# Kernel tuning notes

Measured on AMD Instinct MI355X. Metric: run time of the kernel, lower is better.

The kernel has to match this reference:

```python
import jax, jax.numpy as jnp
import numpy as np
import math

NUM_CLASSES = 722
BLUR_RANGE = 3
# gaussian_val(dist, sigma=1) = exp(-2**dist / (2 * 2**1)) = exp(-2**dist / 4)
DECAYS = [math.exp(-(2.0 ** d) / 4.0) for d in range(BLUR_RANGE + 1)]


def setup_inputs() -> dict:
    key = jax.random.key(0)
    k1, k2 = jax.random.split(key)
    pred = jax.random.normal(k1, (32, 2048, NUM_CLASSES), dtype=jnp.float32)
    target = jax.random.randint(k2, (32, 2048), 0, NUM_CLASSES, dtype=jnp.int32)
    return {"pred": pred, "target": target}


def _smoothed_label(target):
    # target: (b, t) int -> (b, t, C) float32 gaussian-blurred one-hot.
    b, t = target.shape
    bi = jnp.arange(b)[:, None]   # (b, 1)
    ti = jnp.arange(t)[None, :]   # (1, t)
    one_hot = jnp.zeros((b, t, NUM_CLASSES), dtype=jnp.float32)
    # Same scatter order as the torch loop: dist = blur..0, direction +1 then -1;
    # later (smaller-dist) scatters overwrite earlier ones, incl. clamped indices.
    for dist in range(BLUR_RANGE, -1, -1):
        for direction in (1, -1):
            blur_idx = jnp.clip(target + direction * dist, 0, NUM_CLASSES - 1)
            one_hot = one_hot.at[bi, ti, blur_idx].set(DECAYS[dist])
    # to_onehot: exact target position gets 1.0 (overwrites decay[0]).
    one_hot = one_hot.at[bi, ti, target].set(1.0)
    return one_hot


def reference(pred, target):
    # pred: (b, t, C) logits; target: (b, t) class indices.
    pred_logit = jax.nn.log_softmax(pred, axis=-1)
    target_smoothed = _smoothed_label(target)
    target_loss_sum = jnp.sum(-pred_logit * target_smoothed, axis=-1)  # (b, t)
    return jnp.mean(target_loss_sum)
```

## Files before the change

### kernel.cpp

```cpp
#include <hip/hip_runtime.h>
#include <math.h>

#define NC 722
#define NROWS 65536
#define ROWS_PER_BLOCK 32
#define ROWS_PER_WAVE 8

__global__ void init_out_kernel(float* out) {
    if (threadIdx.x == 0) out[0] = 0.0f;
}

__global__ __launch_bounds__(256) void ce_gauss_kernel(
        const float* __restrict__ pred,
        const int* __restrict__ target,
        float* __restrict__ out) {
    const int lane = threadIdx.x & 63;
    const int wave = threadIdx.x >> 6;
    __shared__ float wave_sums[4];

    float acc = 0.0f;
    const int row0 = blockIdx.x * ROWS_PER_BLOCK + wave * ROWS_PER_WAVE;

    for (int r = row0; r < row0 + ROWS_PER_WAVE; ++r) {
        const float* __restrict__ p = pred + (size_t)r * NC;

        float se = 0.0f;
        for (int i = lane; i < NC; i += 64) {
            se += __expf(p[i]);
        }
        #pragma unroll
        for (int off = 32; off > 0; off >>= 1) {
            se += __shfl_xor(se, off, 64);
        }

        if (lane == 0) {
            const int t = target[r];
            float w[7] = {0.f, 0.f, 0.f, 0.f, 0.f, 0.f, 0.f};
            const float dec[4] = {0.778800783071f,
                                  0.606530659713f,
                                  0.367879441171f,
                                  0.135335283237f};
            #pragma unroll
            for (int dist = 3; dist >= 1; --dist) {
                int ip = t + dist; if (ip > NC - 1) ip = NC - 1;
                int im = t - dist; if (im < 0) im = 0;
                w[ip - t + 3] = dec[dist];
                w[im - t + 3] = dec[dist];
            }
            w[3] = 1.0f;

            float sumw = 0.0f, dot = 0.0f;
            #pragma unroll
            for (int j = 0; j < 7; ++j) {
                if (w[j] > 0.0f) {
                    sumw += w[j];
                    dot += w[j] * p[t - 3 + j];
                }
            }
            acc += sumw * __logf(se) - dot;
        }
    }

    if (lane == 0) wave_sums[wave] = acc;
    __syncthreads();
    if (threadIdx.x == 0) {
        float s = wave_sums[0] + wave_sums[1] + wave_sums[2] + wave_sums[3];
        atomicAdd(out, s * (1.0f / (float)NROWS));
    }
}

extern "C" void kernel_launch(void* const* d_in, const int* in_sizes, int n_in,
                              void* d_out, int out_size, void* d_ws, size_t ws_size,
                              hipStream_t stream) {
    const float* pred = (const float*)d_in[0];
    const int* target = (const int*)d_in[1];
    float* out = (float*)d_out;

    init_out_kernel<<<1, 64, 0, stream>>>(out);

    const int grid = NROWS / ROWS_PER_BLOCK;
    ce_gauss_kernel<<<grid, 256, 0, stream>>>(pred, target, out);
}
```

Before: 317.7 us.

## Process four rows per wave concurrently with float2 loads and parallel dot gather

```diff
diff --git a/kernel.cpp b/kernel.cpp
--- a/kernel.cpp
+++ b/kernel.cpp
@@ -2,9 +2,11 @@
 #include <math.h>
 
 #define NC 722
+#define NF2 361
 #define NROWS 65536
-#define ROWS_PER_BLOCK 32
-#define ROWS_PER_WAVE 8
+#define ROWS_PER_WAVE 4
+#define WAVES_PER_BLOCK 4
+#define ROWS_PER_BLOCK (ROWS_PER_WAVE * WAVES_PER_BLOCK)
 
 __global__ void init_out_kernel(float* out) {
     if (threadIdx.x == 0) out[0] = 0.0f;
@@ -16,50 +18,84 @@
         float* __restrict__ out) {
     const int lane = threadIdx.x & 63;
     const int wave = threadIdx.x >> 6;
-    __shared__ float wave_sums[4];
+    __shared__ float wt_lds[WAVES_PER_BLOCK][ROWS_PER_WAVE][8];
+    __shared__ float wave_sums[WAVES_PER_BLOCK];
 
-    float acc = 0.0f;
     const int row0 = blockIdx.x * ROWS_PER_BLOCK + wave * ROWS_PER_WAVE;
 
-    for (int r = row0; r < row0 + ROWS_PER_WAVE; ++r) {
-        const float* __restrict__ p = pred + (size_t)r * NC;
-
-        float se = 0.0f;
-        for (int i = lane; i < NC; i += 64) {
-            se += __expf(p[i]);
+    int   tgt[ROWS_PER_WAVE];
+    float sumw[ROWS_PER_WAVE];
+    const float DEC1 = 0.606530659713f;
+    const float DEC2 = 0.367879441171f;
+    const float DEC3 = 0.135335283237f;
+    #pragma unroll
+    for (int rr = 0; rr < ROWS_PER_WAVE; ++rr) {
+        const int t = target[row0 + rr];
+        tgt[rr] = t;
+        float w[7] = {0.f, 0.f, 0.f, 0.f, 0.f, 0.f, 0.f};
+        #pragma unroll
+        for (int dist = 3; dist >= 1; --dist) {
+            const float dv = (dist == 3) ? DEC3 : (dist == 2) ? DEC2 : DEC1;
+            int ip = t + dist; if (ip > NC - 1) ip = NC - 1;
+            int im = t - dist; if (im < 0) im = 0;
+            w[ip - t + 3] = dv;
+            w[im - t + 3] = dv;
         }
-        #pragma unroll
-        for (int off = 32; off > 0; off >>= 1) {
-            se += __shfl_xor(se, off, 64);
-        }
-
+        w[3] = 1.0f;
+        sumw[rr] = w[0] + w[1] + w[2] + w[3] + w[4] + w[5] + w[6];
         if (lane == 0) {
-            const int t = target[r];
-            float w[7] = {0.f, 0.f, 0.f, 0.f, 0.f, 0.f, 0.f};
-            const float dec[4] = {0.778800783071f,
-                                  0.606530659713f,
-                                  0.367879441171f,
-                                  0.135335283237f};
             #pragma unroll
-            for (int dist = 3; dist >= 1; --dist) {
-                int ip = t + dist; if (ip > NC - 1) ip = NC - 1;
-                int im = t - dist; if (im < 0) im = 0;
-                w[ip - t + 3] = dec[dist];
-                w[im - t + 3] = dec[dist];
-            }
-            w[3] = 1.0f;
-
-            float sumw = 0.0f, dot = 0.0f;
-            #pragma unroll
-            for (int j = 0; j < 7; ++j) {
-                if (w[j] > 0.0f) {
-                    sumw += w[j];
-                    dot += w[j] * p[t - 3 + j];
-                }
-            }
-            acc += sumw * __logf(se) - dot;
+            for (int j = 0; j < 7; ++j) wt_lds[wave][rr][j] = w[j];
         }
     }
+
+    const float2* __restrict__ p2[ROWS_PER_WAVE];
+    #pragma unroll
+    for (int rr = 0; rr < ROWS_PER_WAVE; ++rr)
+        p2[rr] = (const float2*)(pred + (size_t)(row0 + rr) * NC);
+
+    float se[ROWS_PER_WAVE] = {0.f, 0.f, 0.f, 0.f};
+    #pragma unroll
+    for (int k = 0; k < 6; ++k) {
+        const int idx = lane + (k << 6);
+        if (idx < NF2) {
+            float2 v0 = p2[0][idx];
+            float2 v1 = p2[1][idx];
+            float2 v2 = p2[2][idx];
+            float2 v3 = p2[3][idx];
+            se[0] += __expf(v0.x) + __expf(v0.y);
+            se[1] += __expf(v1.x) + __expf(v1.y);
+            se[2] += __expf(v2.x) + __expf(v2.y);
+            se[3] += __expf(v3.x) + __expf(v3.y);
+        }
+    }
+    #pragma unroll
+    for (int rr = 0; rr < ROWS_PER_WAVE; ++rr) {
+        #pragma unroll
+        for (int off = 32; off > 0; off >>= 1)
+            se[rr] += __shfl_xor(se[rr], off, 64);
+    }
+
+    float dotv = 0.f;
+    const int grr = lane >> 3;
+    const int gj  = lane & 7;
+    if (grr < ROWS_PER_WAVE && gj < 7) {
+        const float wv = wt_lds[wave][grr][gj];
+        if (wv > 0.f) {
+            const int c = tgt[grr] - 3 + gj;
+            dotv = wv * pred[(size_t)(row0 + grr) * NC + c];
+        }
+    }
+    dotv += __shfl_xor(dotv, 1, 64);
+    dotv += __shfl_xor(dotv, 2, 64);
+    dotv += __shfl_xor(dotv, 4, 64);
+
+    float acc = 0.f;
+    if (gj == 0 && grr < ROWS_PER_WAVE)
+        acc = sumw[grr] * __logf(se[grr]) - dotv;
+    #pragma unroll
+    for (int off = 32; off > 0; off >>= 1)
+        acc += __shfl_xor(acc, off, 64);
 
     if (lane == 0) wave_sums[wave] = acc;
     __syncthreads();
```

Result: faster. 270.5 us (-14.9%).
